# Kernel tuning notes

Measured on AMD Instinct MI355X. Metric: run time of the kernel, lower is better.

## Reference

```python
import jax, jax.numpy as jnp
import numpy as np

N = 200000
E = 500000
F_IN = 165
HID = 256
N_CLASSES = 2


def setup_inputs() -> dict:
    key = jax.random.key(0)
    ks = jax.random.split(key, 8)
    x = jax.random.normal(ks[0], (N, F_IN), dtype=jnp.float32)
    edge_index = jax.random.randint(ks[1], (2, E), 0, N, dtype=jnp.int64)
    # PyG SAGEConv params: lin_l applied to mean-aggregated neighbors (with bias),
    # lin_r applied to root features (no bias). Glorot-ish init scale.
    def lin(k, fin, fout):
        return jax.random.normal(k, (fin, fout), dtype=jnp.float32) / np.sqrt(fin)
    return {
        "x": x,
        "edge_index": edge_index,
        "w1_l": lin(ks[2], F_IN, HID),
        "w1_r": lin(ks[3], F_IN, HID),
        "b1": jnp.zeros((HID,), dtype=jnp.float32),
        "w2_l": lin(ks[4], HID, N_CLASSES),
        "w2_r": lin(ks[5], HID, N_CLASSES),
        "b2": jnp.zeros((N_CLASSES,), dtype=jnp.float32),
    }


def _sage_conv(x, edge_index, w_l, w_r, b):
    # PyG SAGEConv with default mean aggregation:
    #   out = lin_l(mean_{j in N(i)} x_j) + lin_r(x_i) + b
    src, dst = edge_index[0], edge_index[1]
    n = x.shape[0]
    deg = jax.ops.segment_sum(jnp.ones((src.shape[0],), x.dtype), dst, num_segments=n)
    agg = jax.ops.segment_sum(x[src], dst, num_segments=n)  # [N, F]
    agg = agg / jnp.maximum(deg, 1.0)[:, None]
    return agg @ w_l + x @ w_r + b


def reference(x, edge_index, w1_l, w1_r, b1, w2_l, w2_r, b2):
    h = jax.nn.relu(_sage_conv(x, edge_index, w1_l, w1_r, b1))
    # F.dropout(training=self.training) is identity in eval mode.
    logits = _sage_conv(h, edge_index, w2_l, w2_r, b2)
    return (logits, edge_index)
```

## Files before the change

### kernel.cpp

```cpp
#include <hip/hip_runtime.h>
#include <hip/hip_bf16.h>
#include <hip/hip_fp16.h>

#define N_NODES 200000
#define N_EDGES 500000
#define F_IN    165
#define HID     256
#define SX      192
#define NB      782

typedef float    floatx4 __attribute__((ext_vector_type(4)));
typedef float    floatx4a __attribute__((ext_vector_type(4), aligned(16)));
typedef float    float4u __attribute__((ext_vector_type(4), aligned(4)));
typedef _Float16 half8   __attribute__((ext_vector_type(8)));

__global__ void cast_x_kernel(const float* __restrict__ x, half8* __restrict__ xh8) {
    int idx = blockIdx.x * blockDim.x + threadIdx.x;
    int row = idx / 24;
    int p = idx - row * 24;
    int f0 = p * 8;
    const float* px = x + (long)row * F_IN + f0;
    half8 r;
    if (f0 + 8 <= F_IN) {
        float4u lo = *(const float4u*)px;
        float4u hi = *(const float4u*)(px + 4);
#pragma unroll
        for (int q = 0; q < 4; ++q) r[q] = (_Float16)lo[q];
#pragma unroll
        for (int q = 0; q < 4; ++q) r[4 + q] = (_Float16)hi[q];
    } else {
#pragma unroll
        for (int q = 0; q < 8; ++q)
            r[q] = (f0 + q < F_IN) ? (_Float16)px[q] : (_Float16)0.0f;
    }
    xh8[idx] = r;
}

__global__ void hist_kernel(const int* __restrict__ ei, int* __restrict__ degi) {
    int e = blockIdx.x * blockDim.x + threadIdx.x;
    if (e < N_EDGES) atomicAdd(&degi[ei[N_EDGES + e]], 1);
}

__global__ __launch_bounds__(256) void block_sum_kernel(const int* __restrict__ degi,
                                                        int* __restrict__ bsum) {
    __shared__ int sh[256];
    int t = threadIdx.x, i = blockIdx.x * 256 + t;
    sh[t] = (i < N_NODES) ? degi[i] : 0;
    __syncthreads();
#pragma unroll
    for (int off = 128; off > 0; off >>= 1) {
        if (t < off) sh[t] += sh[t + off];
        __syncthreads();
    }
    if (t == 0) bsum[blockIdx.x] = sh[0];
}

__global__ __launch_bounds__(1024) void scan_bsum_kernel(const int* __restrict__ bsum,
                                                         int* __restrict__ boff,
                                                         int* __restrict__ row_start) {
    __shared__ int sh[1024];
    int t = threadIdx.x;
    int v = (t < NB) ? bsum[t] : 0;
    sh[t] = v;
    __syncthreads();
    for (int off = 1; off < 1024; off <<= 1) {
        int u = (t >= off) ? sh[t - off] : 0;
        __syncthreads();
        sh[t] += u;
        __syncthreads();
    }
    if (t < NB) boff[t] = sh[t] - v;
    if (t == 1023) row_start[N_NODES] = sh[1023];
}

__global__ __launch_bounds__(256) void scan_emit_kernel(const int* __restrict__ degi,
                                                        const int* __restrict__ boff,
                                                        int* __restrict__ row_start,
                                                        int* __restrict__ cursor,
                                                        float* __restrict__ invdeg) {
    __shared__ int sh[256];
    int t = threadIdx.x, i = blockIdx.x * 256 + t;
    int d = (i < N_NODES) ? degi[i] : 0;
    sh[t] = d;
    __syncthreads();
#pragma unroll
    for (int off = 1; off < 256; off <<= 1) {
        int u = (t >= off) ? sh[t - off] : 0;
        __syncthreads();
        sh[t] += u;
        __syncthreads();
    }
    if (i < N_NODES) {
        int row = boff[blockIdx.x] + sh[t] - d;
        row_start[i] = row;
        cursor[i] = row;
        invdeg[i] = 1.0f / fmaxf((float)d, 1.0f);
    }
}

__global__ void scatter_edges_kernel(const int* __restrict__ ei,
                                     int* __restrict__ cursor,
                                     int* __restrict__ csr) {
    int e = blockIdx.x * blockDim.x + threadIdx.x;
    if (e >= N_EDGES) return;
    int s = ei[e];
    int d = ei[N_EDGES + e];
    int pos = atomicAdd(&cursor[d], 1);
    csr[pos] = s;
}

__global__ void gather_agg_kernel(const half8* __restrict__ xh8,
                                  const int* __restrict__ row_start,
                                  const int* __restrict__ csr,
                                  half8* __restrict__ aggh8) {
    int idx = blockIdx.x * blockDim.x + threadIdx.x;
    int n = idx / 24;
    int p = idx - n * 24;
    int e0 = row_start[n], e1 = row_start[n + 1];
    half8 acc = {0, 0, 0, 0, 0, 0, 0, 0};
    half8 acc2 = {0, 0, 0, 0, 0, 0, 0, 0};
    int e = e0;
    for (; e + 2 <= e1; e += 2) {
        int s0 = csr[e], s1 = csr[e + 1];
        half8 v0 = xh8[(long)s0 * 24 + p];
        half8 v1 = xh8[(long)s1 * 24 + p];
        acc += v0;
        acc2 += v1;
    }
    if (e < e1) acc += xh8[(long)csr[e] * 24 + p];
    aggh8[idx] = acc + acc2;
}

__global__ void prep_bfrag_kernel(const float* __restrict__ w1l,
                                  const float* __restrict__ w1r,
                                  _Float16* __restrict__ bfrag) {
    int gid = blockIdx.x * blockDim.x + threadIdx.x;
    if (gid >= 12 * 16 * 64) return;
    int lane = gid & 63;
    int j = (gid >> 6) & 15;
    int c = gid >> 10;
    int quad = lane >> 4, n = lane & 15;
    const float* w = (c < 6) ? w1l : w1r;
    int kb = (c < 6 ? c : c - 6) * 32;
    int col = j * 16 + n;
    half8 r;
#pragma unroll
    for (int q = 0; q < 8; ++q) {
        int k = kb + quad * 8 + q;
        r[q] = (_Float16)((k < F_IN) ? w[k * HID + col] : 0.0f);
    }
    *(half8*)(bfrag + gid * 8) = r;
}

__global__ __launch_bounds__(512, 4) void gemm_fused_kernel(
        const _Float16* __restrict__ xh, const _Float16* __restrict__ aggh,
        const float* __restrict__ invdeg, const _Float16* __restrict__ bfrag,
        const float* __restrict__ b1,
        const float* __restrict__ w2l, const float* __restrict__ w2r,
        float* __restrict__ tl, float* __restrict__ tr) {
    __shared__ __attribute__((aligned(16))) _Float16 As[2][128 * 64];
    __shared__ float tlr[128][4];
    const int tid = threadIdx.x;
    const int w = tid >> 6, lane = tid & 63;
    const int quad = lane >> 4, l15 = lane & 15;
    const int rowbase = blockIdx.x * 128;
    const int rhalf = (w & 1) * 64;
    const int hidg = (w >> 1);

    ((float*)tlr)[tid] = 0.0f;

    const int srow_l = tid >> 2;
    const int sseg = (tid & 3) ^ ((srow_l >> 1) & 3);
    int srow = rowbase + srow_l;
    if (srow >= N_NODES) srow = N_NODES - 1;
    const int sgoff = srow * SX + sseg * 8;
    const int ldst = (tid & ~63) * 16;

    int aoff[4];
#pragma unroll
    for (int nt = 0; nt < 4; ++nt) {
        int r = rhalf + nt * 16 + l15;
        int slot = r * 4 + (quad ^ ((r >> 1) & 3));
        aoff[nt] = slot * 16;
    }
    const int boff = (hidg * 4 * 64 + lane) * 16;

    floatx4 acc[4][4];
#pragma unroll
    for (int i = 0; i < 4; ++i)
#pragma unroll
        for (int nt = 0; nt < 4; ++nt)
            acc[i][nt] = (floatx4){0.f, 0.f, 0.f, 0.f};

    auto STAGE = [&](int p) {
#pragma unroll
        for (int u = 0; u < 2; ++u) {
            const int cc = 2 * p + u;
            const _Float16* src = (cc < 6) ? aggh : xh;
            const int kb = (cc < 6 ? cc : cc - 6) * 32;
            const _Float16* gp = src + sgoff + kb;
            char* dst = (char*)(&As[p & 1][u * 128 * 32]) + ldst;
            __builtin_amdgcn_global_load_lds(
                (const __attribute__((address_space(1))) void*)gp,
                (__attribute__((address_space(3))) void*)dst, 16, 0, 0);
        }
    };

    STAGE(0);
    asm volatile("s_waitcnt vmcnt(0)" ::: "memory");
    __builtin_amdgcn_s_barrier();
    __builtin_amdgcn_sched_barrier(0);

#pragma unroll 1
    for (int t = 0; t < 6; ++t) {
        if (t < 5) STAGE(t + 1);
        const char* abase = (const char*)(&As[t & 1][0]);
#pragma unroll
        for (int u = 0; u < 2; ++u) {
            const int cc = 2 * t + u;
            half8 a[4], b[4];
#pragma unroll
            for (int nt = 0; nt < 4; ++nt)
                a[nt] = *(const half8*)(abase + u * 8192 + aoff[nt]);
#pragma unroll
            for (int i = 0; i < 4; ++i)
                b[i] = *(const half8*)((const char*)bfrag + boff + (cc * 16 + i) * 1024);
#pragma unroll
            for (int i = 0; i < 4; ++i)
#pragma unroll
                for (int nt = 0; nt < 4; ++nt)
                    acc[i][nt] = __builtin_amdgcn_mfma_f32_16x16x32_f16(b[i], a[nt], acc[i][nt], 0, 0, 0);
        }
        if (t == 2) {
#pragma unroll
            for (int nt = 0; nt < 4; ++nt) {
                int r = rowbase + rhalf + nt * 16 + l15;
                float iv = (r < N_NODES) ? invdeg[r] : 0.0f;
#pragma unroll
                for (int i = 0; i < 4; ++i)
                    acc[i][nt] *= iv;
            }
        }
        asm volatile("s_waitcnt vmcnt(0)" ::: "memory");
        __builtin_amdgcn_s_barrier();
        __builtin_amdgcn_sched_barrier(0);
    }

    float s[4][4];
#pragma unroll
    for (int nt = 0; nt < 4; ++nt)
#pragma unroll
        for (int c = 0; c < 4; ++c) s[nt][c] = 0.0f;

#pragma unroll
    for (int i = 0; i < 4; ++i) {
        const int j0 = hidg * 64 + i * 16 + quad * 4;
        floatx4a bbv = *(const floatx4a*)(b1 + j0);
        floatx4a wlA = *(const floatx4a*)(w2l + j0 * 2);
        floatx4a wlB = *(const floatx4a*)(w2l + j0 * 2 + 4);
        floatx4a wrA = *(const floatx4a*)(w2r + j0 * 2);
        floatx4a wrB = *(const floatx4a*)(w2r + j0 * 2 + 4);
#pragma unroll
        for (int nt = 0; nt < 4; ++nt) {
#pragma unroll
            for (int reg = 0; reg < 4; ++reg) {
                float v = fmaxf(acc[i][nt][reg] + bbv[reg], 0.0f);
                float wl0 = (reg < 2) ? wlA[(reg & 1) * 2]     : wlB[(reg & 1) * 2];
                float wl1 = (reg < 2) ? wlA[(reg & 1) * 2 + 1] : wlB[(reg & 1) * 2 + 1];
                float wr0 = (reg < 2) ? wrA[(reg & 1) * 2]     : wrB[(reg & 1) * 2];
                float wr1 = (reg < 2) ? wrA[(reg & 1) * 2 + 1] : wrB[(reg & 1) * 2 + 1];
                s[nt][0] += v * wl0;
                s[nt][1] += v * wl1;
                s[nt][2] += v * wr0;
                s[nt][3] += v * wr1;
            }
        }
    }
#pragma unroll
    for (int nt = 0; nt < 4; ++nt) {
#pragma unroll
        for (int c = 0; c < 4; ++c) {
            s[nt][c] += __shfl_xor(s[nt][c], 16, 64);
            s[nt][c] += __shfl_xor(s[nt][c], 32, 64);
        }
        if (quad == 0) {
            int rl = rhalf + nt * 16 + l15;
            atomicAdd(&tlr[rl][0], s[nt][0]);
            atomicAdd(&tlr[rl][1], s[nt][1]);
            atomicAdd(&tlr[rl][2], s[nt][2]);
            atomicAdd(&tlr[rl][3], s[nt][3]);
        }
    }
    __syncthreads();
    if (tid < 128) {
        int row = rowbase + tid;
        if (row < N_NODES) {
            tl[row * 2 + 0] = tlr[tid][0];
            tl[row * 2 + 1] = tlr[tid][1];
            tr[row * 2 + 0] = tlr[tid][2];
            tr[row * 2 + 1] = tlr[tid][3];
        }
    }
}

__global__ void gather_out_kernel(const int* __restrict__ row_start,
                                  const int* __restrict__ csr,
                                  const float* __restrict__ tl,
                                  const float* __restrict__ tr,
                                  const float* __restrict__ invdeg,
                                  const float* __restrict__ b2,
                                  float* __restrict__ out) {
    int i = blockIdx.x * blockDim.x + threadIdx.x;
    if (i >= N_NODES) return;
    int e0 = row_start[i], e1 = row_start[i + 1];
    float a0 = 0.f, a1 = 0.f;
    for (int e = e0; e < e1; ++e) {
        int s = csr[e];
        a0 += tl[s * 2 + 0];
        a1 += tl[s * 2 + 1];
    }
    float inv = invdeg[i];
    out[i * 2 + 0] = a0 * inv + tr[i * 2 + 0] + b2[0];
    out[i * 2 + 1] = a1 * inv + tr[i * 2 + 1] + b2[1];
}

__global__ void cast_edges_kernel(const int* __restrict__ ei,
                                  float* __restrict__ out) {
    int i = blockIdx.x * blockDim.x + threadIdx.x;
    if (i < 2 * N_EDGES) out[i] = (float)ei[i];
}

extern "C" void kernel_launch(void* const* d_in, const int* in_sizes, int n_in,
                              void* d_out, int out_size, void* d_ws, size_t ws_size,
                              hipStream_t stream) {
    const float* x    = (const float*)d_in[0];
    const int*   ei   = (const int*)d_in[1];
    const float* w1_l = (const float*)d_in[2];
    const float* w1_r = (const float*)d_in[3];
    const float* b1   = (const float*)d_in[4];
    const float* w2_l = (const float*)d_in[5];
    const float* w2_r = (const float*)d_in[6];
    const float* b2   = (const float*)d_in[7];

    char* ws = (char*)d_ws;
    int*   degi      = (int*)(ws);
    int*   row_start = (int*)(ws + 800000);
    int*   cursor    = (int*)(ws + 1600032);
    float* invdeg    = (float*)(ws + 2400032);
    int*   csr       = (int*)(ws + 3200032);
    float* tl        = (float*)(ws + 5200032);
    float* tr        = (float*)(ws + 6800032);
    int*   bsum      = (int*)(ws + 8400032);
    int*   boff      = (int*)(ws + 8403232);
    _Float16* bfrag  = (_Float16*)(ws + 8406432);
    _Float16* aggh   = (_Float16*)(ws + 8610000);
    _Float16* xh     = (_Float16*)(ws + 85410000);

    float* out = (float*)d_out;

    (void)hipMemsetAsync(degi, 0, 800000, stream);

    cast_x_kernel<<<(N_NODES * 24) / 256, 256, 0, stream>>>(x, (half8*)xh);
    prep_bfrag_kernel<<<48, 256, 0, stream>>>(w1_l, w1_r, bfrag);

    hist_kernel<<<(N_EDGES + 255) / 256, 256, 0, stream>>>(ei, degi);
    block_sum_kernel<<<NB, 256, 0, stream>>>(degi, bsum);
    scan_bsum_kernel<<<1, 1024, 0, stream>>>(bsum, boff, row_start);
    scan_emit_kernel<<<NB, 256, 0, stream>>>(degi, boff, row_start, cursor, invdeg);
    scatter_edges_kernel<<<(N_EDGES + 255) / 256, 256, 0, stream>>>(ei, cursor, csr);

    gather_agg_kernel<<<(N_NODES * 24) / 256, 256, 0, stream>>>(
        (const half8*)xh, row_start, csr, (half8*)aggh);

    gemm_fused_kernel<<<(N_NODES + 127) / 128, 512, 0, stream>>>(
        xh, aggh, invdeg, bfrag, b1, w2_l, w2_r, tl, tr);

    gather_out_kernel<<<NB, 256, 0, stream>>>(row_start, csr, tl, tr, invdeg, b2, out);
    cast_edges_kernel<<<(2 * N_EDGES + 255) / 256, 256, 0, stream>>>(ei, out + 2 * N_NODES);
}
```

Before: 429.3 us.

## Load A fragments directly from global memory instead of LDS double-buffering

Removes the LDS double-buffered staging of the A tiles (aggregated and root features), which used global_load_lds with barriers. Each wave now reads its half8 A fragments straight from global memory at per-row offsets. This drops LDS usage and per-step barriers, but every wave covering the same rows re-reads the same A data from global or L2, and loads are no longer overlapped with the MFMA work of the previous step.

```diff
diff --git a/kernel.cpp b/kernel.cpp
--- a/kernel.cpp
+++ b/kernel.cpp
@@ -158,7 +158,6 @@
         const float* __restrict__ b1,
         const float* __restrict__ w2l, const float* __restrict__ w2r,
         float* __restrict__ tl, float* __restrict__ tr) {
-    __shared__ __attribute__((aligned(16))) _Float16 As[2][128 * 64];
     __shared__ float tlr[128][4];
     const int tid = threadIdx.x;
     const int w = tid >> 6, lane = tid & 63;
@@ -168,20 +167,14 @@
     const int hidg = (w >> 1);
 
     ((float*)tlr)[tid] = 0.0f;
-
-    const int srow_l = tid >> 2;
-    const int sseg = (tid & 3) ^ ((srow_l >> 1) & 3);
-    int srow = rowbase + srow_l;
-    if (srow >= N_NODES) srow = N_NODES - 1;
-    const int sgoff = srow * SX + sseg * 8;
-    const int ldst = (tid & ~63) * 16;
+    __syncthreads();
 
     int aoff[4];
 #pragma unroll
     for (int nt = 0; nt < 4; ++nt) {
-        int r = rhalf + nt * 16 + l15;
-        int slot = r * 4 + (quad ^ ((r >> 1) & 3));
-        aoff[nt] = slot * 16;
+        int r = rowbase + rhalf + nt * 16 + l15;
+        if (r >= N_NODES) r = N_NODES - 1;
+        aoff[nt] = r * SX + quad * 8;
     }
     const int boff = (hidg * 4 * 64 + lane) * 16;
 
@@ -192,36 +185,17 @@
         for (int nt = 0; nt < 4; ++nt)
             acc[i][nt] = (floatx4){0.f, 0.f, 0.f, 0.f};
 
-    auto STAGE = [&](int p) {
-#pragma unroll
-        for (int u = 0; u < 2; ++u) {
-            const int cc = 2 * p + u;
-            const _Float16* src = (cc < 6) ? aggh : xh;
-            const int kb = (cc < 6 ? cc : cc - 6) * 32;
-            const _Float16* gp = src + sgoff + kb;
-            char* dst = (char*)(&As[p & 1][u * 128 * 32]) + ldst;
-            __builtin_amdgcn_global_load_lds(
-                (const __attribute__((address_space(1))) void*)gp,
-                (__attribute__((address_space(3))) void*)dst, 16, 0, 0);
-        }
-    };
-
-    STAGE(0);
-    asm volatile("s_waitcnt vmcnt(0)" ::: "memory");
-    __builtin_amdgcn_s_barrier();
-    __builtin_amdgcn_sched_barrier(0);
-
 #pragma unroll 1
     for (int t = 0; t < 6; ++t) {
-        if (t < 5) STAGE(t + 1);
-        const char* abase = (const char*)(&As[t & 1][0]);
 #pragma unroll
         for (int u = 0; u < 2; ++u) {
             const int cc = 2 * t + u;
+            const _Float16* __restrict__ src = (cc < 6) ? aggh : xh;
+            const int kb = (cc < 6 ? cc : cc - 6) * 32;
             half8 a[4], b[4];
 #pragma unroll
             for (int nt = 0; nt < 4; ++nt)
-                a[nt] = *(const half8*)(abase + u * 8192 + aoff[nt]);
+                a[nt] = *(const half8*)(src + aoff[nt] + kb);
 #pragma unroll
             for (int i = 0; i < 4; ++i)
                 b[i] = *(const half8*)((const char*)bfrag + boff + (cc * 16 + i) * 1024);
@@ -241,9 +215,6 @@
                     acc[i][nt] *= iv;
             }
         }
-        asm volatile("s_waitcnt vmcnt(0)" ::: "memory");
-        __builtin_amdgcn_s_barrier();
-        __builtin_amdgcn_sched_barrier(0);
     }
 
     float s[4][4];
```

Result: slower. 472.0 us (+10.0%).
